# Kernel tuning notes

Hardware: AMD Instinct MI355X
Metric: run time of the kernel (lower is better)

## Reference

```python
import jax, jax.numpy as jnp
import numpy as np
from jax import lax

H, W = 480, 320
BS, PAD, SF, WIN = 20, 6, 4, 32        # block, zero-pad, scale, window = BS+2*PAD
NH, NW = H // BS, W // BS              # 24, 16 -> 384 blocks


def _conv(x, w, b, stride=1, pad=0):
    out = lax.conv_general_dilated(x, w, (stride, stride), [(pad, pad), (pad, pad)],
                                   dimension_numbers=('NCHW', 'OIHW', 'NCHW'))
    return out + b[None, :, None, None]


def _rep_conv(x, w, b):  # 3x3 conv with replicate padding (padding_mode='replicate')
    xp = jnp.pad(x, ((0, 0), (0, 0), (1, 1), (1, 1)), mode='edge')
    return _conv(xp, w, b)


def _maxpool2(x):
    return lax.reduce_window(x, -jnp.inf, lax.max, (1, 1, 2, 2), (1, 1, 2, 2), 'VALID')


def _pixel_shuffle(x, r=SF):  # (N, C*r*r, h, w) -> (N, C, h*r, w*r), torch ordering
    n, crr, h, w = x.shape
    c = crr // (r * r)
    return x.reshape(n, c, r, r, h, w).transpose(0, 1, 4, 2, 5, 3).reshape(n, c, h * r, w * r)


def _he(key, shape):
    std = np.sqrt(2.0 / (shape[0] * shape[2] * shape[3]))
    return jax.random.normal(key, shape, jnp.float32) * std


def setup_inputs() -> dict:
    key = jax.random.key(0)
    ks = jax.random.split(key, 16)
    return {
        'x': jax.random.normal(ks[0], (1, 3, H, W), jnp.float32),
        'cls_w1': _he(ks[1], (32, 3, 3, 3)),  'cls_b1': jnp.zeros((32,), jnp.float32),
        'cls_w2': _he(ks[2], (32, 32, 3, 3)), 'cls_b2': jnp.zeros((32,), jnp.float32),
        'cls_w3': _he(ks[3], (16, 32, 3, 3)), 'cls_b3': jnp.zeros((16,), jnp.float32),
        'cls_w4': _he(ks[4], (8, 16, 3, 3)),  'cls_b4': jnp.zeros((8,), jnp.float32),
        'cls_w5': _he(ks[5], (1, 8, 5, 5)),   'cls_b5': jnp.zeros((1,), jnp.float32),
        'lt_w1': _he(ks[6], (16, 3, 3, 3)),   'lt_b1': jnp.zeros((16,), jnp.float32),
        'lt_w2': _he(ks[7], (48, 16, 3, 3)),  'lt_b2': jnp.zeros((48,), jnp.float32),
        'cx_w1': _he(ks[8], (64, 3, 3, 3)),   'cx_b1': jnp.zeros((64,), jnp.float32),
        'cx_w2': _he(ks[9], (64, 64, 3, 3)),  'cx_b2': jnp.zeros((64,), jnp.float32),
        'cx_w3': _he(ks[10], (48, 64, 3, 3)), 'cx_b3': jnp.zeros((48,), jnp.float32),
    }


def reference(x, cls_w1, cls_b1, cls_w2, cls_b2, cls_w3, cls_b3, cls_w4, cls_b4,
              cls_w5, cls_b5, lt_w1, lt_b1, lt_w2, lt_b2,
              cx_w1, cx_b1, cx_w2, cx_b2, cx_w3, cx_b3):
    relu = jax.nn.relu
    # ---- classifier (gate) ----
    h = relu(_rep_conv(x, cls_w1, cls_b1))
    h = _maxpool2(relu(_rep_conv(h, cls_w2, cls_b2)))
    h = relu(_rep_conv(h, cls_w3, cls_b3))
    h = _maxpool2(relu(_rep_conv(h, cls_w4, cls_b4)))
    h = _conv(h, cls_w5, cls_b5, stride=BS // 4)          # (1,1,NH,NW)
    class_vector = jax.nn.sigmoid(h.reshape(-1))          # (NH*NW,)

    # ---- blockify (overlapping 32x32 windows, stride 20, zero pad 6) ----
    xp = jnp.pad(x, ((0, 0), (0, 0), (PAD, PAD), (PAD, PAD)))
    hidx = jnp.arange(NH)[:, None] * BS + jnp.arange(WIN)
    widx = jnp.arange(NW)[:, None] * BS + jnp.arange(WIN)
    t = xp[:, :, hidx]
    t = t[:, :, :, :, widx]
    blocks = t.transpose(0, 2, 4, 1, 3, 5).reshape(NH * NW, 3, WIN, WIN)

    # ---- experts (run on all blocks; mask-select == one-hot gather/scatter) ----
    lt = _pixel_shuffle(_conv(relu(_conv(blocks, lt_w1, lt_b1, pad=1)), lt_w2, lt_b2, pad=1))
    lt = jnp.clip(lt, 0.0, 1.0)
    cx = relu(_conv(blocks, cx_w1, cx_b1, pad=1))
    cx = relu(_conv(cx, cx_w2, cx_b2, pad=1))
    cx = jnp.clip(_pixel_shuffle(_conv(cx, cx_w3, cx_b3, pad=1)), 0.0, 1.0)

    is_complex = class_vector > 0.5
    out = jnp.where(is_complex[:, None, None, None], cx, lt)  # (N,3,128,128)

    # ---- crop halo and reassemble full image ----
    c0 = SF * PAD
    out = out[:, :, c0:c0 + SF * BS, c0:c0 + SF * BS]          # (N,3,80,80)
    img = out.reshape(NH, NW, 3, SF * BS, SF * BS)
    img = img.transpose(2, 0, 3, 1, 4).reshape(1, 3, NH * SF * BS, NW * SF * BS)
    return img, class_vector
```

## Files before the change

### kernel.cpp

```cpp
#include <hip/hip_runtime.h>
#include <hip/hip_bf16.h>
#include <math.h>

static constexpr int H = 480, W = 320, NH = 24, NW = 16, NB = 384;
static constexpr int HW = H * W;
static constexpr int H2 = 240, W2 = 160;
static constexpr int HW2 = H2 * W2;
static constexpr int H4 = 120, W4 = 80;
static constexpr int HW4 = H4 * W4;
static constexpr int IMG_PIX = 3 * 1920 * 1280;

typedef __attribute__((ext_vector_type(8))) short short8;
typedef __attribute__((ext_vector_type(4))) float f32x4;
typedef __attribute__((ext_vector_type(8))) unsigned short ushort8;

static constexpr int WQ_CX2 = 0;
static constexpr int WQ_CX3 = 36864;
static constexpr int WQ_LT2 = 64512;
static constexpr int WQ_FCX = 78336;
static constexpr int WQ_FLT = 80384;
static constexpr int WQ_CLS2 = 80896;
static constexpr int WPK_ALL = 108544;

__device__ __forceinline__ int iclamp(int v, int lo, int hi) {
    return v < lo ? lo : (v > hi ? hi : v);
}
__device__ __forceinline__ unsigned short f2bfu(float x) {
    __hip_bfloat16 h = __float2bfloat16(x);
    return *reinterpret_cast<unsigned short*>(&h);
}
__device__ __forceinline__ float bf2f(unsigned short u) {
    __hip_bfloat16 h = *reinterpret_cast<__hip_bfloat16*>(&u);
    return __bfloat162float(h);
}


__global__ __launch_bounds__(256) void k_pack(const float* __restrict__ cx_w2,
                                              const float* __restrict__ cx_w3,
                                              const float* __restrict__ lt_w2,
                                              const float* __restrict__ cx_w1,
                                              const float* __restrict__ lt_w1,
                                              const float* __restrict__ cls_w2,
                                              unsigned short* __restrict__ wpk) {
    int i = blockIdx.x * 256 + threadIdx.x;
    if (i >= WPK_ALL) return;
    float v = 0.f;
    if (i < WQ_CX3) {
        int c = i >> 9, r = i & 511;
        int lane = r >> 3, j = r & 7;
        int col = lane & 15, kq = lane >> 4;
        int nt = c & 3, kc = (c >> 2) & 1, t = c >> 3;
        int co = nt * 16 + col, ci = kc * 32 + kq * 8 + j;
        v = cx_w2[(co * 64 + ci) * 9 + t];
    } else if (i < WQ_LT2) {
        int c = (i - WQ_CX3) >> 9, r = i & 511;
        int lane = r >> 3, j = r & 7;
        int col = lane & 15, kq = lane >> 4;
        int nt = c % 3, q = c / 3;
        int kc = q & 1, t = q >> 1;
        int co = nt * 16 + col, ci = kc * 32 + kq * 8 + j;
        v = cx_w3[(co * 64 + ci) * 9 + t];
    } else if (i < WQ_FCX) {
        int c = (i - WQ_LT2) >> 9, r = i & 511;
        int lane = r >> 3, j = r & 7;
        int col = lane & 15, kq = lane >> 4;
        int nt = c % 3, t = c / 3;
        int co = nt * 16 + col, ci = kq * 8 + j;
        v = (ci < 16) ? lt_w2[(co * 16 + ci) * 9 + t] : 0.f;
    } else if (i < WQ_FLT) {
        int c = (i - WQ_FCX) >> 9, r = i & 511;
        int lane = r >> 3, j = r & 7;
        int col = lane & 15, kq = lane >> 4;
        int co = c * 16 + col, k = kq * 8 + j;
        v = (k < 27) ? cx_w1[co * 27 + k] : 0.f;
    } else if (i < WQ_CLS2) {
        int r = i & 511;
        int lane = r >> 3, j = r & 7;
        int col = lane & 15, kq = lane >> 4;
        int k = kq * 8 + j;
        v = (k < 27) ? lt_w1[col * 27 + k] : 0.f;
    } else {
        int c = (i - WQ_CLS2) >> 9, r = i & 511;
        int lane = r >> 3, j = r & 7;
        int col = lane & 15, kq = lane >> 4;
        int nt = c & 1, q = c >> 1;
        int t = q % 9, pl = q / 9;
        int co = nt * 16 + col, ci = kq * 8 + j;
        float w = cls_w2[(co * 32 + ci) * 9 + t];
        unsigned short h = f2bfu(w);
        float r1 = w - bf2f(h);
        unsigned short m = f2bfu(r1);
        unsigned short l = f2bfu(r1 - bf2f(m));
        wpk[i] = pl == 0 ? h : (pl == 1 ? m : l);
        return;
    }
    wpk[i] = f2bfu(v);
}


__global__ __launch_bounds__(256) void k_cls1s(const float* __restrict__ x,
                                               const float* __restrict__ w,
                                               const float* __restrict__ b,
                                               unsigned short* __restrict__ c1s) {
    int p = blockIdx.x * 256 + threadIdx.x;
    if (p >= HW) return;
    int coc = blockIdx.y;
    int y = p / W, xx = p - y * W;
    float in[27];
#pragma unroll
    for (int ci = 0; ci < 3; ++ci)
#pragma unroll
        for (int dy = 0; dy < 3; ++dy) {
            int yy = iclamp(y + dy - 1, 0, H - 1);
#pragma unroll
            for (int dx = 0; dx < 3; ++dx) {
                int xc = iclamp(xx + dx - 1, 0, W - 1);
                in[ci * 9 + dy * 3 + dx] = x[ci * HW + yy * W + xc];
            }
        }
    ushort8 hv, mv, lv;
#pragma unroll
    for (int c8 = 0; c8 < 8; ++c8) {
        int co = coc * 8 + c8;
        float acc = b[co];
#pragma unroll
        for (int k = 0; k < 27; ++k) acc = fmaf(w[co * 27 + k], in[k], acc);
        float v = fmaxf(acc, 0.f);
        unsigned short h = f2bfu(v);
        float r1 = v - bf2f(h);
        unsigned short m = f2bfu(r1);
        unsigned short l = f2bfu(r1 - bf2f(m));
        hv[c8] = h; mv[c8] = m; lv[c8] = l;
    }
    *(ushort8*)(c1s + (long)p * 32 + coc * 8) = hv;
    *(ushort8*)(c1s + (long)32 * HW + (long)p * 32 + coc * 8) = mv;
    *(ushort8*)(c1s + (long)64 * HW + (long)p * 32 + coc * 8) = lv;
}

template <int P>
__device__ __forceinline__ void cls2_phase(const unsigned short* __restrict__ src,
                                           unsigned short* __restrict__ sh2,
                                           const unsigned short* __restrict__ wb,
                                           f32x4 acc[4][2], int tid, int ty, int tx) {
    int lane = tid & 63, wave = tid >> 6;
    int col = lane & 15, kq = lane >> 4;
    __syncthreads();
    for (int idx = tid; idx < 1296; idx += 256) {
        int pix = idx >> 2, g = idx & 3;
        int hy = iclamp(ty * 16 + pix / 18 - 1, 0, H - 1);
        int hx = iclamp(tx * 16 + pix % 18 - 1, 0, W - 1);
        ushort8 v = *(const ushort8*)(src + ((long)(hy * W + hx)) * 32 + g * 8);
        *(ushort8*)(sh2 + pix * 32 + ((g ^ ((pix >> 1) & 3)) * 8)) = v;
    }
    __syncthreads();
#pragma unroll
    for (int t = 0; t < 9; ++t) {
        int dy = t / 3, dx = t - dy * 3;
        short8 B[2][P];
#pragma unroll
        for (int nt = 0; nt < 2; ++nt)
#pragma unroll
            for (int pl = 0; pl < P; ++pl)
                B[nt][pl] = *(const short8*)(wb + ((pl * 9 + t) * 2 + nt) * 512 + lane * 8);
#pragma unroll
        for (int i = 0; i < 4; ++i) {
            int pix = (wave * 4 + i + dy) * 18 + col + dx;
            short8 a = *(const short8*)(sh2 + pix * 32 + ((kq ^ ((pix >> 1) & 3)) * 8));
#pragma unroll
            for (int nt = 0; nt < 2; ++nt)
#pragma unroll
                for (int pl = 0; pl < P; ++pl)
                    acc[i][nt] = __builtin_amdgcn_mfma_f32_16x16x32_bf16(a, B[nt][pl],
                                                                         acc[i][nt], 0, 0, 0);
        }
    }
}

__global__ __launch_bounds__(256, 2) void k_cls2m(const unsigned short* __restrict__ c1s,
                                                  const unsigned short* __restrict__ wpk,
                                                  const float* __restrict__ b2,
                                                  float* __restrict__ c2) {
    extern __shared__ unsigned short sh2[];
    int tid = threadIdx.x;
    int tile = blockIdx.x;
    int ty = tile / 20, tx = tile - ty * 20;
    int lane = tid & 63, wave = tid >> 6;
    int col = lane & 15, kq = lane >> 4;
    const unsigned short* wb = wpk + WQ_CLS2;
    f32x4 acc[4][2];
#pragma unroll
    for (int nt = 0; nt < 2; ++nt) {
        float bv = b2[nt * 16 + col];
#pragma unroll
        for (int i = 0; i < 4; ++i) acc[i][nt] = f32x4{bv, bv, bv, bv};
    }
    cls2_phase<3>(c1s, sh2, wb, acc, tid, ty, tx);
    cls2_phase<2>(c1s + (long)32 * HW, sh2, wb + 18 * 512, acc, tid, ty, tx);
    cls2_phase<1>(c1s + (long)64 * HW, sh2, wb + 36 * 512, acc, tid, ty, tx);
    __syncthreads();
    float* pool = (float*)sh2;
#pragma unroll
    for (int i = 0; i < 4; ++i)
#pragma unroll
        for (int nt = 0; nt < 2; ++nt)
#pragma unroll
            for (int rr = 0; rr < 4; ++rr)
                pool[(nt * 16 + col) * 257 + (wave * 4 + i) * 16 + kq * 4 + rr] =
                    fmaxf(acc[i][nt][rr], 0.f);
    __syncthreads();
#pragma unroll
    for (int k = 0; k < 8; ++k) {
        int o = tid + k * 256;
        int co = o >> 6, rem = o & 63;
        int py = rem >> 3, px = rem & 7;
        const float* lp = pool + co * 257 + py * 32 + px * 2;
        float m = fmaxf(fmaxf(lp[0], lp[1]), fmaxf(lp[16], lp[17]));
        c2[co * HW2 + (ty * 8 + py) * W2 + tx * 8 + px] = m;
    }
}

__global__ __launch_bounds__(256) void k_cls3(const float* __restrict__ in,
                                              const float* __restrict__ w,
                                              const float* __restrict__ b,
                                              float* __restrict__ p3) {
    int p = blockIdx.x * 256 + threadIdx.x;
    if (p >= HW2) return;
    int cc = blockIdx.y;
    int s = blockIdx.z;
    int y = p / W2, xx = p - y * W2;
    float acc[8];
#pragma unroll
    for (int co = 0; co < 8; ++co) acc[co] = s ? 0.f : b[cc * 8 + co];
    for (int cil = 0; cil < 16; ++cil) {
        int ci = s * 16 + cil;
        float v[9];
#pragma unroll
        for (int dy = 0; dy < 3; ++dy) {
            int yy = iclamp(y + dy - 1, 0, H2 - 1);
#pragma unroll
            for (int dx = 0; dx < 3; ++dx) {
                int xc = iclamp(xx + dx - 1, 0, W2 - 1);
                v[dy * 3 + dx] = in[ci * HW2 + yy * W2 + xc];
            }
        }
#pragma unroll
        for (int co = 0; co < 8; ++co)
#pragma unroll
            for (int k = 0; k < 9; ++k)
                acc[co] = fmaf(w[(cc * 8 + co) * 288 + ci * 9 + k], v[k], acc[co]);
    }
#pragma unroll
    for (int co = 0; co < 8; ++co) p3[(s * 16 + cc * 8 + co) * HW2 + p] = acc[co];
}

__global__ __launch_bounds__(256) void k_cls4f(const float* __restrict__ p3,
                                               const float* __restrict__ w,
                                               const float* __restrict__ b,
                                               float* __restrict__ out) {
    __shared__ float lds[8 * 256];
    int t = threadIdx.x;
    int tile = blockIdx.x;
    int ty = tile / 10, tx = tile - ty * 10;
    int ly = t >> 4, lx = t & 15;
    int y = ty * 16 + ly, xx = tx * 16 + lx;
    float acc[8];
#pragma unroll
    for (int co = 0; co < 8; ++co) acc[co] = b[co];
    for (int ci = 0; ci < 16; ++ci) {
        float v[9];
#pragma unroll
        for (int dy = 0; dy < 3; ++dy) {
            int yy = iclamp(y + dy - 1, 0, H2 - 1);
#pragma unroll
            for (int dx = 0; dx < 3; ++dx) {
                int xc = iclamp(xx + dx - 1, 0, W2 - 1);
                int idx = ci * HW2 + yy * W2 + xc;
                v[dy * 3 + dx] = fmaxf(p3[idx] + p3[idx + 16 * HW2], 0.f);
            }
        }
#pragma unroll
        for (int co = 0; co < 8; ++co) {
            const float* wp = w + co * 144 + ci * 9;
#pragma unroll
            for (int k = 0; k < 9; ++k) acc[co] = fmaf(wp[k], v[k], acc[co]);
        }
    }
#pragma unroll
    for (int co = 0; co < 8; ++co) lds[co * 256 + t] = fmaxf(acc[co], 0.f);
    __syncthreads();
#pragma unroll
    for (int k = 0; k < 2; ++k) {
        int o = t + k * 256;
        int co = o >> 6, rem = o & 63;
        int py = rem >> 3, px = rem & 7;
        const float* lp = lds + co * 256 + py * 32 + px * 2;
        float m = fmaxf(fmaxf(lp[0], lp[1]), fmaxf(lp[16], lp[17]));
        out[co * HW4 + (ty * 8 + py) * W4 + tx * 8 + px] = m;
    }
}

__global__ __launch_bounds__(64) void k_cls5(const float* __restrict__ in,
                                             const float* __restrict__ w,
                                             const float* __restrict__ b,
                                             float* __restrict__ clsv,
                                             float* __restrict__ out_cls) {
    int bidx = blockIdx.x;
    int oy = bidx / NW, ox = bidx - oy * NW;
    int lane = threadIdx.x;
    float s = 0.f;
    for (int k = lane; k < 200; k += 64) {
        int ci = k / 25, r = k - ci * 25;
        int ky = r / 5, kx = r - ky * 5;
        s = fmaf(w[k], in[ci * HW4 + (oy * 5 + ky) * W4 + (ox * 5 + kx)], s);
    }
#pragma unroll
    for (int off = 32; off; off >>= 1) s += __shfl_down(s, off, 64);
    if (lane == 0) {
        float sig = 1.f / (1.f + expf(-(s + b[0])));
        clsv[bidx] = sig;
        out_cls[bidx] = sig;
    }
}

__global__ __launch_bounds__(512)
__attribute__((amdgpu_waves_per_eu(4, 4)))
void k_block(const float* __restrict__ x,
             const unsigned short* __restrict__ wpk,
             const float* __restrict__ lt_b1,
             const float* __restrict__ cx_b1,
             const float* __restrict__ lt_b2,
             const float* __restrict__ cx_b2,
             const float* __restrict__ cx_b3,
             const float* __restrict__ clsv,
             float* __restrict__ out) {
    extern __shared__ unsigned short sh[];
    unsigned short* T1 = sh;
    unsigned short* T2 = sh + 16384;
    unsigned short* XH = sh + 28672;
    int wg = blockIdx.x;
    int b = wg / 5, e = wg - b * 5;
    bool cx = clsv[b] > 0.5f;
    int bh = b / NW, bw = b - bh * NW;
    int base = 6 + 4 * e;
    int tid = threadIdx.x;
    int lane = tid & 63, wave = tid >> 6;
    int col = lane & 15, kq = lane >> 4;

    if (!cx) {
        ushort8 z = {0, 0, 0, 0, 0, 0, 0, 0};
        for (int i = tid; i < 1024; i += 512) *(ushort8*)(T1 + i * 8) = z;
    }
    if (tid < 340) {
        int xr = tid / 34, xcc = tid - xr * 34;
        int yg = bh * 20 + (base - 3 + xr) - 6;
        int xg = bw * 20 + (xcc - 1) - 6;
        bool ok = (unsigned)yg < (unsigned)H && (unsigned)xg < (unsigned)W;
#pragma unroll
        for (int ci = 0; ci < 3; ++ci)
            XH[ci * 340 + tid] = ok ? f2bfu(x[ci * HW + yg * W + xg])
                                    : (unsigned short)0;
    }
    __syncthreads();

    if (cx) {
        short8 Bf[4];
        float bv[4];
#pragma unroll
        for (int nt = 0; nt < 4; ++nt) {
            Bf[nt] = *(const short8*)(wpk + WQ_FCX + nt * 512 + lane * 8);
            bv[nt] = cx_b1[nt * 16 + col];
        }
#pragma unroll
        for (int i = 0; i < 2; ++i) {
            int mt = wave + 8 * i;
            int tr = mt >> 1, xc0 = (mt & 1) << 4;
            short8 av;
#pragma unroll
            for (int j = 0; j < 8; ++j) {
                int k = kq * 8 + j;
                int kk = k < 27 ? k : 0;
                int ci = kk / 9, t = kk - ci * 9;
                int dy = t / 3, dx = t - dy * 3;
                unsigned short v = XH[ci * 340 + (tr + dy) * 34 + (xc0 + col + dx)];
                av[j] = (k < 27) ? (short)v : (short)0;
            }
#pragma unroll
            for (int nt = 0; nt < 4; ++nt) {
                f32x4 acc = {bv[nt], bv[nt], bv[nt], bv[nt]};
                acc = __builtin_amdgcn_mfma_f32_16x16x32_bf16(av, Bf[nt], acc, 0, 0, 0);
                int co = nt * 16 + col;
#pragma unroll
                for (int r = 0; r < 4; ++r) {
                    int p1 = mt * 16 + kq * 4 + r;
                    T1[p1 * 64 + (((co >> 3) ^ (p1 & 7)) << 3) + (co & 7)] =
                        f2bfu(fmaxf(acc[r], 0.f));
                }
            }
        }
    } else {
        short8 Bf = *(const short8*)(wpk + WQ_FLT + lane * 8);
        float bv = lt_b1[col];
#pragma unroll
        for (int i = 0; i < 2; ++i) {
            int mt = wave + 8 * i;
            int tr = mt >> 1, xc0 = (mt & 1) << 4;
            short8 av;
#pragma unroll
            for (int j = 0; j < 8; ++j) {
                int k = kq * 8 + j;
                int kk = k < 27 ? k : 0;
                int ci = kk / 9, t = kk - ci * 9;
                int dy = t / 3, dx = t - dy * 3;
                unsigned short v = XH[ci * 340 + (tr + dy) * 34 + (xc0 + col + dx)];
                av[j] = (k < 27) ? (short)v : (short)0;
            }
            f32x4 acc = {bv, bv, bv, bv};
            acc = __builtin_amdgcn_mfma_f32_16x16x32_bf16(av, Bf, acc, 0, 0, 0);
#pragma unroll
            for (int r = 0; r < 4; ++r) {
                int p1 = mt * 16 + kq * 4 + r;
                T1[p1 * 32 + (((col >> 3) ^ ((p1 >> 1) & 3)) << 3) + (col & 7)] =
                    f2bfu(fmaxf(acc[r], 0.f));
            }
        }
    }
    __syncthreads();

    if (cx) {
        {
            f32x4 acc[2][4];
#pragma unroll
            for (int nt = 0; nt < 4; ++nt) {
                float bv = cx_b2[nt * 16 + col];
#pragma unroll
                for (int i = 0; i < 2; ++i) acc[i][nt] = f32x4{bv, bv, bv, bv};
            }
#pragma unroll
            for (int t = 0; t < 9; ++t) {
                int dy = t / 3, dx = t - dy * 3;
                short8 B[4][2];
#pragma unroll
                for (int nt = 0; nt < 4; ++nt)
#pragma unroll
                    for (int kc = 0; kc < 2; ++kc)
                        B[nt][kc] = *(const short8*)(wpk + WQ_CX2 +
                                                     ((t * 2 + kc) * 4 + nt) * 512 +
                                                     lane * 8);
#pragma unroll
                for (int i = 0; i < 2; ++i) {
                    int mt = wave + 8 * i;
                    if (mt >= 12) continue;
                    int tr = (mt >> 1) + dy;
                    int xs = ((mt & 1) << 4) + col + dx - 1;
                    bool xv = (unsigned)xs < 32u;
                    int xcl = xs < 0 ? 0 : (xs > 31 ? 31 : xs);
                    int p1 = tr * 32 + xcl;
#pragma unroll
                    for (int kc = 0; kc < 2; ++kc) {
                        int c = kc * 4 + kq;
                        short8 a = *(const short8*)(T1 + p1 * 64 + ((c ^ (p1 & 7)) << 3));
                        if (!xv) a = short8{0, 0, 0, 0, 0, 0, 0, 0};
#pragma unroll
                        for (int nt = 0; nt < 4; ++nt)
                            acc[i][nt] = __builtin_amdgcn_mfma_f32_16x16x32_bf16(
                                a, B[nt][kc], acc[i][nt], 0, 0, 0);
                    }
                }
            }
#pragma unroll
            for (int i = 0; i < 2; ++i) {
                int mt = wave + 8 * i;
                if (mt >= 12) continue;
#pragma unroll
                for (int nt = 0; nt < 4; ++nt) {
                    int co = nt * 16 + col;
#pragma unroll
                    for (int r = 0; r < 4; ++r) {
                        int p2 = mt * 16 + kq * 4 + r;
                        T2[p2 * 64 + (((co >> 3) ^ (p2 & 7)) << 3) + (co & 7)] =
                            f2bfu(fmaxf(acc[i][nt][r], 0.f));
                    }
                }
            }
        }
        __syncthreads();
        {
            int mt = wave;
            f32x4 acc[3];
#pragma unroll
            for (int nt = 0; nt < 3; ++nt) {
                float bv = cx_b3[nt * 16 + col];
                acc[nt] = f32x4{bv, bv, bv, bv};
            }
#pragma unroll
            for (int t = 0; t < 9; ++t) {
                int dy = t / 3, dx = t - dy * 3;
                short8 B[3][2];
#pragma unroll
                for (int nt = 0; nt < 3; ++nt)
#pragma unroll
                    for (int kc = 0; kc < 2; ++kc)
                        B[nt][kc] = *(const short8*)(wpk + WQ_CX3 +
                                                     ((t * 2 + kc) * 3 + nt) * 512 +
                                                     lane * 8);
                int tr2 = (mt >> 1) + dy;
                int xs = ((mt & 1) << 4) + col + dx - 1;
                bool xv = (unsigned)xs < 32u;
                int xcl = xs < 0 ? 0 : (xs > 31 ? 31 : xs);
                int p2 = tr2 * 32 + xcl;
#pragma unroll
                for (int kc = 0; kc < 2; ++kc) {
                    int c = kc * 4 + kq;
                    short8 a = *(const short8*)(T2 + p2 * 64 + ((c ^ (p2 & 7)) << 3));
                    if (!xv) a = short8{0, 0, 0, 0, 0, 0, 0, 0};
#pragma unroll
                    for (int nt = 0; nt < 3; ++nt)
                        acc[nt] = __builtin_amdgcn_mfma_f32_16x16x32_bf16(
                            a, B[nt][kc], acc[nt], 0, 0, 0);
                }
            }
            int py = base + (mt >> 1);
#pragma unroll
            for (int nt = 0; nt < 3; ++nt) {
                int co = nt * 16 + col;
                int ch = co >> 4, dy2 = (co >> 2) & 3, dx2 = co & 3;
#pragma unroll
                for (int r = 0; r < 4; ++r) {
                    int p = mt * 16 + kq * 4 + r;
                    int px = p & 31;
                    int s0 = px * 4 + dx2 - 24;
                    if ((unsigned)s0 < 80u) {
                        int r0 = py * 4 + dy2 - 24;
                        float v = fminf(fmaxf(acc[nt][r], 0.f), 1.f);
                        out[ch * 2457600 + (bh * 80 + r0) * 1280 + bw * 80 + s0] = v;
                    }
                }
            }
        }
    } else {
        int mt = wave;
        f32x4 acc[3];
#pragma unroll
        for (int nt = 0; nt < 3; ++nt) {
            float bv = lt_b2[nt * 16 + col];
            acc[nt] = f32x4{bv, bv, bv, bv};
        }
#pragma unroll
        for (int t = 0; t < 9; ++t) {
            int dy = t / 3, dx = t - dy * 3;
            short8 B[3];
#pragma unroll
            for (int nt = 0; nt < 3; ++nt)
                B[nt] = *(const short8*)(wpk + WQ_LT2 + (t * 3 + nt) * 512 + lane * 8);
            int tr = (mt >> 1) + 1 + dy;
            int xs = ((mt & 1) << 4) + col + dx - 1;
            bool xv = (unsigned)xs < 32u;
            int xcl = xs < 0 ? 0 : (xs > 31 ? 31 : xs);
            int p1 = tr * 32 + xcl;
            short8 a = *(const short8*)(T1 + p1 * 32 + ((kq ^ ((p1 >> 1) & 3)) << 3));
            if (!xv) a = short8{0, 0, 0, 0, 0, 0, 0, 0};
#pragma unroll
            for (int nt = 0; nt < 3; ++nt)
                acc[nt] = __builtin_amdgcn_mfma_f32_16x16x32_bf16(a, B[nt], acc[nt], 0, 0, 0);
        }
        int py = base + (mt >> 1);
#pragma unroll
        for (int nt = 0; nt < 3; ++nt) {
            int co = nt * 16 + col;
            int ch = co >> 4, dy2 = (co >> 2) & 3, dx2 = co & 3;
#pragma unroll
            for (int r = 0; r < 4; ++r) {
                int p = mt * 16 + kq * 4 + r;
                int px = p & 31;
                int s0 = px * 4 + dx2 - 24;
                if ((unsigned)s0 < 80u) {
                    int r0 = py * 4 + dy2 - 24;
                    float v = fminf(fmaxf(acc[nt][r], 0.f), 1.f);
                    out[ch * 2457600 + (bh * 80 + r0) * 1280 + bw * 80 + s0] = v;
                }
            }
        }
    }
}

extern "C" void kernel_launch(void* const* d_in, const int* in_sizes, int n_in,
                              void* d_out, int out_size, void* d_ws, size_t ws_size,
                              hipStream_t stream) {
    const float* x      = (const float*)d_in[0];
    const float* cls_w1 = (const float*)d_in[1];
    const float* cls_b1 = (const float*)d_in[2];
    const float* cls_w2 = (const float*)d_in[3];
    const float* cls_b2 = (const float*)d_in[4];
    const float* cls_w3 = (const float*)d_in[5];
    const float* cls_b3 = (const float*)d_in[6];
    const float* cls_w4 = (const float*)d_in[7];
    const float* cls_b4 = (const float*)d_in[8];
    const float* cls_w5 = (const float*)d_in[9];
    const float* cls_b5 = (const float*)d_in[10];
    const float* lt_w1  = (const float*)d_in[11];
    const float* lt_b1  = (const float*)d_in[12];
    const float* lt_w2  = (const float*)d_in[13];
    const float* lt_b2  = (const float*)d_in[14];
    const float* cx_w1  = (const float*)d_in[15];
    const float* cx_b1  = (const float*)d_in[16];
    const float* cx_w2  = (const float*)d_in[17];
    const float* cx_b2  = (const float*)d_in[18];
    const float* cx_w3  = (const float*)d_in[19];
    const float* cx_b3  = (const float*)d_in[20];

    float* ws = (float*)d_ws;
    float* out = (float*)d_out;

    size_t off = 0;
    float* c2 = ws + off;   off += (size_t)32 * HW2;
    float* c4 = ws + off;   off += (size_t)8 * HW4;
    float* clsv = ws + off; off += 384;
    unsigned short* wpk = (unsigned short*)(ws + off); off += (WPK_ALL + 1) / 2;
    size_t fixed = off;

    unsigned short* c1s = (unsigned short*)(ws + fixed);
    float* p3 = ws + fixed + (size_t)48 * HW;

    (void)hipFuncSetAttribute((const void*)k_cls2m,
                              hipFuncAttributeMaxDynamicSharedMemorySize, 32896);
    (void)hipFuncSetAttribute((const void*)k_block,
                              hipFuncAttributeMaxDynamicSharedMemorySize, 59384);

    k_pack<<<(WPK_ALL + 255) / 256, 256, 0, stream>>>(cx_w2, cx_w3, lt_w2, cx_w1, lt_w1,
                                                      cls_w2, wpk);
    k_cls1s<<<dim3((HW + 255) / 256, 4), 256, 0, stream>>>(x, cls_w1, cls_b1, c1s);
    k_cls2m<<<600, 256, 32896, stream>>>(c1s, wpk, cls_b2, c2);
    k_cls3<<<dim3(150, 2, 2), 256, 0, stream>>>(c2, cls_w3, cls_b3, p3);
    k_cls4f<<<150, 256, 0, stream>>>(p3, cls_w4, cls_b4, c4);
    k_cls5<<<NB, 64, 0, stream>>>(c4, cls_w5, cls_b5, clsv, out + IMG_PIX);
    k_block<<<NB * 5, 512, 59384, stream>>>(x, wpk, lt_b1, cx_b1, lt_b2, cx_b2,
                                            cx_b3, clsv, out);
}
```

Baseline: 175.5 us.

## Split each block into ten two-row strips and spread output channels across waves

Each image block is now processed by 10 workgroups of two output rows each, instead of 5 workgroups of four rows. Shared memory shrinks, so more workgroups can be resident per CU, and the waves-per-EU cap is raised. The final conv's 48 output channels are split so that waves 0-3 handle 32 channels and waves 4-7 handle the remaining 16, which rebalances the MFMA work across all eight waves. In exchange, the halo recompute for the earlier layers grows because the strips are shorter, and twice as many workgroups are launched.

```diff
diff --git a/kernel.cpp b/kernel.cpp
--- a/kernel.cpp
+++ b/kernel.cpp
@@ -323,7 +323,7 @@
 }
 
 __global__ __launch_bounds__(512)
-__attribute__((amdgpu_waves_per_eu(4, 4)))
+__attribute__((amdgpu_waves_per_eu(4, 8)))
 void k_block(const float* __restrict__ x,
              const unsigned short* __restrict__ wpk,
              const float* __restrict__ lt_b1,
@@ -335,29 +335,29 @@
              float* __restrict__ out) {
     extern __shared__ unsigned short sh[];
     unsigned short* T1 = sh;
-    unsigned short* T2 = sh + 16384;
-    unsigned short* XH = sh + 28672;
+    unsigned short* T2 = sh + 12288;
+    unsigned short* XH = sh + 20480;
     int wg = blockIdx.x;
-    int b = wg / 5, e = wg - b * 5;
+    int b = wg / 10, e = wg - b * 10;
     bool cx = clsv[b] > 0.5f;
     int bh = b / NW, bw = b - bh * NW;
-    int base = 6 + 4 * e;
+    int base = 6 + 2 * e;
     int tid = threadIdx.x;
     int lane = tid & 63, wave = tid >> 6;
     int col = lane & 15, kq = lane >> 4;
 
     if (!cx) {
         ushort8 z = {0, 0, 0, 0, 0, 0, 0, 0};
-        for (int i = tid; i < 1024; i += 512) *(ushort8*)(T1 + i * 8) = z;
-    }
-    if (tid < 340) {
+        for (int i = tid; i < 768; i += 512) *(ushort8*)(T1 + i * 8) = z;
+    }
+    if (tid < 272) {
         int xr = tid / 34, xcc = tid - xr * 34;
         int yg = bh * 20 + (base - 3 + xr) - 6;
         int xg = bw * 20 + (xcc - 1) - 6;
         bool ok = (unsigned)yg < (unsigned)H && (unsigned)xg < (unsigned)W;
 #pragma unroll
         for (int ci = 0; ci < 3; ++ci)
-            XH[ci * 340 + tid] = ok ? f2bfu(x[ci * HW + yg * W + xg])
+            XH[ci * 272 + tid] = ok ? f2bfu(x[ci * HW + yg * W + xg])
                                     : (unsigned short)0;
     }
     __syncthreads();
@@ -373,6 +373,7 @@
 #pragma unroll
         for (int i = 0; i < 2; ++i) {
             int mt = wave + 8 * i;
+            if (mt >= 12) break;
             int tr = mt >> 1, xc0 = (mt & 1) << 4;
             short8 av;
 #pragma unroll
@@ -381,7 +382,7 @@
                 int kk = k < 27 ? k : 0;
                 int ci = kk / 9, t = kk - ci * 9;
                 int dy = t / 3, dx = t - dy * 3;
-                unsigned short v = XH[ci * 340 + (tr + dy) * 34 + (xc0 + col + dx)];
+                unsigned short v = XH[ci * 272 + (tr + dy) * 34 + (xc0 + col + dx)];
                 av[j] = (k < 27) ? (short)v : (short)0;
             }
 #pragma unroll
@@ -403,6 +404,7 @@
 #pragma unroll
         for (int i = 0; i < 2; ++i) {
             int mt = wave + 8 * i;
+            if (mt >= 12) break;
             int tr = mt >> 1, xc0 = (mt & 1) << 4;
             short8 av;
 #pragma unroll
@@ -411,7 +413,7 @@
                 int kk = k < 27 ? k : 0;
                 int ci = kk / 9, t = kk - ci * 9;
                 int dy = t / 3, dx = t - dy * 3;
-                unsigned short v = XH[ci * 340 + (tr + dy) * 34 + (xc0 + col + dx)];
+                unsigned short v = XH[ci * 272 + (tr + dy) * 34 + (xc0 + col + dx)];
                 av[j] = (k < 27) ? (short)v : (short)0;
             }
             f32x4 acc = {bv, bv, bv, bv};
@@ -428,12 +430,13 @@
 
     if (cx) {
         {
-            f32x4 acc[2][4];
+            int mt = wave;
+            int sr = mt >> 1;
+            f32x4 acc[4];
 #pragma unroll
             for (int nt = 0; nt < 4; ++nt) {
                 float bv = cx_b2[nt * 16 + col];
-#pragma unroll
-                for (int i = 0; i < 2; ++i) acc[i][nt] = f32x4{bv, bv, bv, bv};
+                acc[nt] = f32x4{bv, bv, bv, bv};
             }
 #pragma unroll
             for (int t = 0; t < 9; ++t) {
@@ -446,82 +449,164 @@
                         B[nt][kc] = *(const short8*)(wpk + WQ_CX2 +
                                                      ((t * 2 + kc) * 4 + nt) * 512 +
                                                      lane * 8);
-#pragma unroll
-                for (int i = 0; i < 2; ++i) {
-                    int mt = wave + 8 * i;
-                    if (mt >= 12) continue;
-                    int tr = (mt >> 1) + dy;
+                int tr = sr + dy;
+                int xs = ((mt & 1) << 4) + col + dx - 1;
+                bool xv = (unsigned)xs < 32u;
+                int xcl = xs < 0 ? 0 : (xs > 31 ? 31 : xs);
+                int p1 = tr * 32 + xcl;
+#pragma unroll
+                for (int kc = 0; kc < 2; ++kc) {
+                    int c = kc * 4 + kq;
+                    short8 a = *(const short8*)(T1 + p1 * 64 + ((c ^ (p1 & 7)) << 3));
+                    if (!xv) a = short8{0, 0, 0, 0, 0, 0, 0, 0};
+#pragma unroll
+                    for (int nt = 0; nt < 4; ++nt)
+                        acc[nt] = __builtin_amdgcn_mfma_f32_16x16x32_bf16(
+                            a, B[nt][kc], acc[nt], 0, 0, 0);
+                }
+            }
+#pragma unroll
+            for (int nt = 0; nt < 4; ++nt) {
+                int co = nt * 16 + col;
+#pragma unroll
+                for (int r = 0; r < 4; ++r) {
+                    int p2 = mt * 16 + kq * 4 + r;
+                    T2[p2 * 64 + (((co >> 3) ^ (p2 & 7)) << 3) + (co & 7)] =
+                        f2bfu(fmaxf(acc[nt][r], 0.f));
+                }
+            }
+        }
+        __syncthreads();
+        {
+            int mt = wave & 3;
+            int o = mt >> 1;
+            if (wave < 4) {
+                f32x4 acc[2];
+#pragma unroll
+                for (int nt = 0; nt < 2; ++nt) {
+                    float bv = cx_b3[nt * 16 + col];
+                    acc[nt] = f32x4{bv, bv, bv, bv};
+                }
+#pragma unroll
+                for (int t = 0; t < 9; ++t) {
+                    int dy = t / 3, dx = t - dy * 3;
+                    short8 B[2][2];
+#pragma unroll
+                    for (int nt = 0; nt < 2; ++nt)
+#pragma unroll
+                        for (int kc = 0; kc < 2; ++kc)
+                            B[nt][kc] = *(const short8*)(wpk + WQ_CX3 +
+                                                         ((t * 2 + kc) * 3 + nt) * 512 +
+                                                         lane * 8);
+                    int tr2 = o + dy;
                     int xs = ((mt & 1) << 4) + col + dx - 1;
                     bool xv = (unsigned)xs < 32u;
                     int xcl = xs < 0 ? 0 : (xs > 31 ? 31 : xs);
-                    int p1 = tr * 32 + xcl;
+                    int p2 = tr2 * 32 + xcl;
 #pragma unroll
                     for (int kc = 0; kc < 2; ++kc) {
                         int c = kc * 4 + kq;
-                        short8 a = *(const short8*)(T1 + p1 * 64 + ((c ^ (p1 & 7)) << 3));
+                        short8 a = *(const short8*)(T2 + p2 * 64 + ((c ^ (p2 & 7)) << 3));
                         if (!xv) a = short8{0, 0, 0, 0, 0, 0, 0, 0};
 #pragma unroll
-                        for (int nt = 0; nt < 4; ++nt)
-                            acc[i][nt] = __builtin_amdgcn_mfma_f32_16x16x32_bf16(
-                                a, B[nt][kc], acc[i][nt], 0, 0, 0);
+                        for (int nt = 0; nt < 2; ++nt)
+                            acc[nt] = __builtin_amdgcn_mfma_f32_16x16x32_bf16(
+                                a, B[nt][kc], acc[nt], 0, 0, 0);
                     }
                 }
-            }
-#pragma unroll
-            for (int i = 0; i < 2; ++i) {
-                int mt = wave + 8 * i;
-                if (mt >= 12) continue;
-#pragma unroll
-                for (int nt = 0; nt < 4; ++nt) {
+                int py = base + o;
+#pragma unroll
+                for (int nt = 0; nt < 2; ++nt) {
                     int co = nt * 16 + col;
+                    int ch = co >> 4, dy2 = (co >> 2) & 3, dx2 = co & 3;
 #pragma unroll
                     for (int r = 0; r < 4; ++r) {
-                        int p2 = mt * 16 + kq * 4 + r;
-                        T2[p2 * 64 + (((co >> 3) ^ (p2 & 7)) << 3) + (co & 7)] =
-                            f2bfu(fmaxf(acc[i][nt][r], 0.f));
+                        int p = mt * 16 + kq * 4 + r;
+                        int px = p & 31;
+                        int s0 = px * 4 + dx2 - 24;
+                        if ((unsigned)s0 < 80u) {
+                            int r0 = py * 4 + dy2 - 24;
+                            float v = fminf(fmaxf(acc[nt][r], 0.f), 1.f);
+                            out[ch * 2457600 + (bh * 80 + r0) * 1280 + bw * 80 + s0] = v;
+                        }
                     }
                 }
-            }
-        }
-        __syncthreads();
-        {
-            int mt = wave;
-            f32x4 acc[3];
-#pragma unroll
-            for (int nt = 0; nt < 3; ++nt) {
-                float bv = cx_b3[nt * 16 + col];
+            } else {
+                f32x4 acc1;
+                {
+                    float bv = cx_b3[32 + col];
+                    acc1 = f32x4{bv, bv, bv, bv};
+                }
+#pragma unroll
+                for (int t = 0; t < 9; ++t) {
+                    int dy = t / 3, dx = t - dy * 3;
+                    short8 B[2];
+#pragma unroll
+                    for (int kc = 0; kc < 2; ++kc)
+                        B[kc] = *(const short8*)(wpk + WQ_CX3 +
+                                                 ((t * 2 + kc) * 3 + 2) * 512 + lane * 8);
+                    int tr2 = o + dy;
+                    int xs = ((mt & 1) << 4) + col + dx - 1;
+                    bool xv = (unsigned)xs < 32u;
+                    int xcl = xs < 0 ? 0 : (xs > 31 ? 31 : xs);
+                    int p2 = tr2 * 32 + xcl;
+#pragma unroll
+                    for (int kc = 0; kc < 2; ++kc) {
+                        int c = kc * 4 + kq;
+                        short8 a = *(const short8*)(T2 + p2 * 64 + ((c ^ (p2 & 7)) << 3));
+                        if (!xv) a = short8{0, 0, 0, 0, 0, 0, 0, 0};
+                        acc1 = __builtin_amdgcn_mfma_f32_16x16x32_bf16(a, B[kc], acc1,
+                                                                       0, 0, 0);
+                    }
+                }
+                int py = base + o;
+                int co = 32 + col;
+                int ch = co >> 4, dy2 = (co >> 2) & 3, dx2 = co & 3;
+#pragma unroll
+                for (int r = 0; r < 4; ++r) {
+                    int p = mt * 16 + kq * 4 + r;
+                    int px = p & 31;
+                    int s0 = px * 4 + dx2 - 24;
+                    if ((unsigned)s0 < 80u) {
+                        int r0 = py * 4 + dy2 - 24;
+                        float v = fminf(fmaxf(acc1[r], 0.f), 1.f);
+                        out[ch * 2457600 + (bh * 80 + r0) * 1280 + bw * 80 + s0] = v;
+                    }
+                }
+            }
+        }
+    } else {
+        int mt = wave & 3;
+        int o = mt >> 1;
+        if (wave < 4) {
+            f32x4 acc[2];
+#pragma unroll
+            for (int nt = 0; nt < 2; ++nt) {
+                float bv = lt_b2[nt * 16 + col];
                 acc[nt] = f32x4{bv, bv, bv, bv};
             }
 #pragma unroll
             for (int t = 0; t < 9; ++t) {
                 int dy = t / 3, dx = t - dy * 3;
-                short8 B[3][2];
-#pragma unroll
-                for (int nt = 0; nt < 3; ++nt)
-#pragma unroll
-                    for (int kc = 0; kc < 2; ++kc)
-                        B[nt][kc] = *(const short8*)(wpk + WQ_CX3 +
-                                                     ((t * 2 + kc) * 3 + nt) * 512 +
-                                                     lane * 8);
-                int tr2 = (mt >> 1) + dy;
+                short8 B[2];
+#pragma unroll
+                for (int nt = 0; nt < 2; ++nt)
+                    B[nt] = *(const short8*)(wpk + WQ_LT2 + (t * 3 + nt) * 512 + lane * 8);
+                int tr = o + dy + 1;
                 int xs = ((mt & 1) << 4) + col + dx - 1;
                 bool xv = (unsigned)xs < 32u;
                 int xcl = xs < 0 ? 0 : (xs > 31 ? 31 : xs);
-                int p2 = tr2 * 32 + xcl;
-#pragma unroll
-                for (int kc = 0; kc < 2; ++kc) {
-                    int c = kc * 4 + kq;
-                    short8 a = *(const short8*)(T2 + p2 * 64 + ((c ^ (p2 & 7)) << 3));
-                    if (!xv) a = short8{0, 0, 0, 0, 0, 0, 0, 0};
-#pragma unroll
-                    for (int nt = 0; nt < 3; ++nt)
-                        acc[nt] = __builtin_amdgcn_mfma_f32_16x16x32_bf16(
-                            a, B[nt][kc], acc[nt], 0, 0, 0);
-                }
-            }
-            int py = base + (mt >> 1);
-#pragma unroll
-            for (int nt = 0; nt < 3; ++nt) {
+                int p1 = tr * 32 + xcl;
+                short8 a = *(const short8*)(T1 + p1 * 32 + ((kq ^ ((p1 >> 1) & 3)) << 3));
+                if (!xv) a = short8{0, 0, 0, 0, 0, 0, 0, 0};
+#pragma unroll
+                for (int nt = 0; nt < 2; ++nt)
+                    acc[nt] = __builtin_amdgcn_mfma_f32_16x16x32_bf16(a, B[nt], acc[nt],
+                                                                      0, 0, 0);
+            }
+            int py = base + o;
+#pragma unroll
+            for (int nt = 0; nt < 2; ++nt) {
                 int co = nt * 16 + col;
                 int ch = co >> 4, dy2 = (co >> 2) & 3, dx2 = co & 3;
 #pragma unroll
@@ -536,37 +621,27 @@
                     }
                 }
             }
-        }
-    } else {
-        int mt = wave;
-        f32x4 acc[3];
-#pragma unroll
-        for (int nt = 0; nt < 3; ++nt) {
-            float bv = lt_b2[nt * 16 + col];
-            acc[nt] = f32x4{bv, bv, bv, bv};
-        }
-#pragma unroll
-        for (int t = 0; t < 9; ++t) {
-            int dy = t / 3, dx = t - dy * 3;
-            short8 B[3];
-#pragma unroll
-            for (int nt = 0; nt < 3; ++nt)
-                B[nt] = *(const short8*)(wpk + WQ_LT2 + (t * 3 + nt) * 512 + lane * 8);
-            int tr = (mt >> 1) + 1 + dy;
-            int xs = ((mt & 1) << 4) + col + dx - 1;
-            bool xv = (unsigned)xs < 32u;
-            int xcl = xs < 0 ? 0 : (xs > 31 ? 31 : xs);
-            int p1 = tr * 32 + xcl;
-            short8 a = *(const short8*)(T1 + p1 * 32 + ((kq ^ ((p1 >> 1) & 3)) << 3));
-            if (!xv) a = short8{0, 0, 0, 0, 0, 0, 0, 0};
-#pragma unroll
-            for (int nt = 0; nt < 3; ++nt)
-                acc[nt] = __builtin_amdgcn_mfma_f32_16x16x32_bf16(a, B[nt], acc[nt], 0, 0, 0);
-        }
-        int py = base + (mt >> 1);
-#pragma unroll
-        for (int nt = 0; nt < 3; ++nt) {
-            int co = nt * 16 + col;
+        } else {
+            f32x4 acc1;
+            {
+                float bv = lt_b2[32 + col];
+                acc1 = f32x4{bv, bv, bv, bv};
+            }
+#pragma unroll
+            for (int t = 0; t < 9; ++t) {
+                int dy = t / 3, dx = t - dy * 3;
+                short8 B = *(const short8*)(wpk + WQ_LT2 + (t * 3 + 2) * 512 + lane * 8);
+                int tr = o + dy + 1;
+                int xs = ((mt & 1) << 4) + col + dx - 1;
+                bool xv = (unsigned)xs < 32u;
+                int xcl = xs < 0 ? 0 : (xs > 31 ? 31 : xs);
+                int p1 = tr * 32 + xcl;
+                short8 a = *(const short8*)(T1 + p1 * 32 + ((kq ^ ((p1 >> 1) & 3)) << 3));
+                if (!xv) a = short8{0, 0, 0, 0, 0, 0, 0, 0};
+                acc1 = __builtin_amdgcn_mfma_f32_16x16x32_bf16(a, B, acc1, 0, 0, 0);
+            }
+            int py = base + o;
+            int co = 32 + col;
             int ch = co >> 4, dy2 = (co >> 2) & 3, dx2 = co & 3;
 #pragma unroll
             for (int r = 0; r < 4; ++r) {
@@ -575,7 +650,7 @@
                 int s0 = px * 4 + dx2 - 24;
                 if ((unsigned)s0 < 80u) {
                     int r0 = py * 4 + dy2 - 24;
-                    float v = fminf(fmaxf(acc[nt][r], 0.f), 1.f);
+                    float v = fminf(fmaxf(acc1[r], 0.f), 1.f);
                     out[ch * 2457600 + (bh * 80 + r0) * 1280 + bw * 80 + s0] = v;
                 }
             }
@@ -624,7 +699,7 @@
     (void)hipFuncSetAttribute((const void*)k_cls2m,
                               hipFuncAttributeMaxDynamicSharedMemorySize, 32896);
     (void)hipFuncSetAttribute((const void*)k_block,
-                              hipFuncAttributeMaxDynamicSharedMemorySize, 59384);
+                              hipFuncAttributeMaxDynamicSharedMemorySize, 42592);
 
     k_pack<<<(WPK_ALL + 255) / 256, 256, 0, stream>>>(cx_w2, cx_w3, lt_w2, cx_w1, lt_w1,
                                                       cls_w2, wpk);
@@ -633,6 +708,6 @@
     k_cls3<<<dim3(150, 2, 2), 256, 0, stream>>>(c2, cls_w3, cls_b3, p3);
     k_cls4f<<<150, 256, 0, stream>>>(p3, cls_w4, cls_b4, c4);
     k_cls5<<<NB, 64, 0, stream>>>(c4, cls_w5, cls_b5, clsv, out + IMG_PIX);
-    k_block<<<NB * 5, 512, 59384, stream>>>(x, wpk, lt_b1, cx_b1, lt_b2, cx_b2,
-                                            cx_b3, clsv, out);
-}
+    k_block<<<NB * 10, 512, 42592, stream>>>(x, wpk, lt_b1, cx_b1, lt_b2, cx_b2,
+                                             cx_b3, clsv, out);
+}
```

New measurement: 203.4 us. +15.9%, slower.
